# Optimization experiments

Measured on AMD Instinct MI355X. Metric: run time of the kernel, lower is better.

The kernel has to match this reference:

```python
import jax, jax.numpy as jnp
import numpy as np

MOMENTUM = 0.9
COMMITMENT_COST = 0.25
EPS = 1e-20


def setup_inputs() -> dict:
    key = jax.random.key(0)
    k1, k2 = jax.random.split(key)
    D, K = 512, 8192
    B, S = 16, 512
    x = jax.random.normal(k1, (B, S, D), dtype=jnp.float32)
    # variance_scaling(1.0, 'fan_in', 'uniform') on shape (D, K): fan_in = D
    limit = np.sqrt(3.0 / D).astype(np.float32)
    e = jax.random.uniform(k2, (D, K), dtype=jnp.float32, minval=-limit, maxval=limit)
    cs = jnp.zeros((K,), dtype=jnp.float32)
    un = jnp.zeros((D, K), dtype=jnp.float32)
    return {"x": x, "e": e, "cs": cs, "un": un}


def reference(x, e, cs, un):
    D, K = e.shape
    input_shape = x.shape[:-1]            # (B, S)
    xf = x.reshape(-1, D)                 # (N, D)
    # pairwise squared distances: (N, K)
    dist = (jnp.sum(xf * xf, axis=1, keepdims=True)
            + jnp.sum(e * e, axis=0, keepdims=True)
            - 2.0 * xf @ e)
    enc_idx = jnp.argmax(-dist, axis=1)                      # (N,)
    enc = jax.nn.one_hot(enc_idx, K, dtype=x.dtype)          # (N, K)
    quantized = jnp.take(e.T, enc_idx, axis=0).reshape(*input_shape, D)

    # EMA codebook update (train=True branch)
    new_cs = (1.0 - MOMENTUM) * jnp.sum(enc, axis=0) + MOMENTUM * cs
    new_un = (1.0 - MOMENTUM) * (xf.T @ enc) + MOMENTUM * un
    n = jnp.sum(new_cs)
    stable_cs = (new_cs + EPS) / (n + K * EPS) * n
    new_e = new_un / stable_cs[None, :]

    loss = COMMITMENT_COST * jnp.mean((jax.lax.stop_gradient(quantized) - x) ** 2)
    quantized_st = x + jax.lax.stop_gradient(quantized - x)  # straight-through

    avg_probs = jnp.mean(enc.reshape(*input_shape, K), axis=0)           # (S, K)
    over_latents = jnp.mean(avg_probs, axis=tuple(range(len(input_shape) - 1)))  # (K,)
    perplexity = jnp.exp(-jnp.sum(over_latents * jnp.log(over_latents + EPS)))
    return quantized_st, loss, perplexity, enc_idx, new_e, new_cs, new_un
```

## Files before the change

kernel.cpp:

```cpp
#include <hip/hip_runtime.h>
#include <math.h>

#define D_ 512
#define K_ 8192
#define N_ 8192
#define KSLICES 8
#define TAU 0.01f

typedef _Float16 f16x8 __attribute__((ext_vector_type(8)));
typedef __attribute__((ext_vector_type(4))) float f32x4;

__global__ void x2_kernel(const float* __restrict__ x, float* __restrict__ x2f) {
    int n = blockIdx.x * 256 + threadIdx.x;
    const float* row = &x[(size_t)n * D_];
    float b[4];
    #pragma unroll
    for (int blk = 0; blk < 4; ++blk) {
        const float* a = row + blk * 128;
        float r[8];
        #pragma unroll
        for (int j = 0; j < 8; ++j) { float v = a[j]; r[j] = __fmul_rn(v, v); }
        for (int i = 8; i < 128; i += 8) {
            #pragma unroll
            for (int j = 0; j < 8; ++j) {
                float v = a[i + j];
                r[j] = __fadd_rn(r[j], __fmul_rn(v, v));
            }
        }
        b[blk] = __fadd_rn(__fadd_rn(__fadd_rn(r[0], r[1]), __fadd_rn(r[2], r[3])),
                           __fadd_rn(__fadd_rn(r[4], r[5]), __fadd_rn(r[6], r[7])));
    }
    x2f[n] = __fadd_rn(__fadd_rn(b[0], b[1]), __fadd_rn(b[2], b[3]));
}

__global__ void e2f_kernel(const float* __restrict__ e, float* __restrict__ e2f) {
    int k = blockIdx.x * 256 + threadIdx.x;
    float s = 0.0f;
    for (int d = 0; d < D_; ++d) {
        float v = e[(size_t)d * K_ + k];
        s = __fadd_rn(s, __fmul_rn(v, v));
    }
    e2f[k] = s;
}

__global__ void xcvt_kernel(const float* __restrict__ x, _Float16* __restrict__ xf) {
    size_t i = ((size_t)blockIdx.x * 256 + threadIdx.x) * 8;
    float4 a = *(const float4*)&x[i];
    float4 b = *(const float4*)&x[i + 4];
    f16x8 h;
    h[0] = (_Float16)a.x; h[1] = (_Float16)a.y; h[2] = (_Float16)a.z; h[3] = (_Float16)a.w;
    h[4] = (_Float16)b.x; h[5] = (_Float16)b.y; h[6] = (_Float16)b.z; h[7] = (_Float16)b.w;
    *(f16x8*)&xf[i] = h;
}

__global__ void ecvtT_kernel(const float* __restrict__ e, _Float16* __restrict__ efT) {
    __shared__ float t[64][65];
    const int tid = threadIdx.x;
    const int k0 = blockIdx.x * 64;
    const int d0 = blockIdx.y * 64;
    #pragma unroll
    for (int it = 0; it < 4; ++it) {
        int dt = (tid >> 4) + it * 16;
        int c4 = (tid & 15) * 4;
        float4 v = *(const float4*)&e[(size_t)(d0 + dt) * K_ + k0 + c4];
        t[dt][c4 + 0] = v.x; t[dt][c4 + 1] = v.y; t[dt][c4 + 2] = v.z; t[dt][c4 + 3] = v.w;
    }
    __syncthreads();
    const int m = tid >> 2, ch = tid & 3;
    f16x8 h0, h1;
    #pragma unroll
    for (int j = 0; j < 8; ++j) h0[j] = (_Float16)t[ch * 16 + j][m];
    #pragma unroll
    for (int j = 0; j < 8; ++j) h1[j] = (_Float16)t[ch * 16 + 8 + j][m];
    size_t o = (size_t)(k0 + m) * D_ + d0 + ch * 16;
    *(f16x8*)&efT[o] = h0;
    *(f16x8*)&efT[o + 8] = h1;
}

__global__ void etrans_kernel(const float* __restrict__ e, float* __restrict__ eT) {
    __shared__ float t[64][65];
    const int tid = threadIdx.x;
    const int k0 = blockIdx.x * 64;
    const int d0 = blockIdx.y * 64;
    #pragma unroll
    for (int it = 0; it < 4; ++it) {
        int dt = (tid >> 4) + it * 16;
        int c4 = (tid & 15) * 4;
        float4 v = *(const float4*)&e[(size_t)(d0 + dt) * K_ + k0 + c4];
        t[dt][c4 + 0] = v.x; t[dt][c4 + 1] = v.y; t[dt][c4 + 2] = v.z; t[dt][c4 + 3] = v.w;
    }
    __syncthreads();
    const int m = tid >> 2, ch = tid & 3;
    size_t o = (size_t)(k0 + m) * D_ + d0 + ch * 16;
    #pragma unroll
    for (int j4 = 0; j4 < 4; ++j4) {
        float4 w;
        w.x = t[ch * 16 + j4 * 4 + 0][m];
        w.y = t[ch * 16 + j4 * 4 + 1][m];
        w.z = t[ch * 16 + j4 * 4 + 2][m];
        w.w = t[ch * 16 + j4 * 4 + 3][m];
        *(float4*)&eT[o + j4 * 4] = w;
    }
}

__launch_bounds__(256, 2)
__global__ void argmin_mfma(const _Float16* __restrict__ xf, const _Float16* __restrict__ efT,
                            const float* __restrict__ x2f, const float* __restrict__ e2f,
                            float* __restrict__ pv4, int* __restrict__ pi4) {
    __shared__ _Float16 XS[2][4096];
    __shared__ _Float16 ES[2][8192];
    __shared__ float e2s[256];

    const int tid = threadIdx.x;
    const int lane = tid & 63;
    const int wid = tid >> 6;
    const int wm = wid & 1, wn = wid >> 1;
    const int lidx = lane & 15, g = lane >> 4;
    const int rowbase = blockIdx.y * 128;
    const int kslice = blockIdx.x;

    float x2r[4];
    #pragma unroll
    for (int nt = 0; nt < 4; ++nt)
        x2r[nt] = x2f[rowbase + (wn << 6) + (nt << 4) + lidx];

    float best[4], sec[4]; int bi[4], si[4];
    #pragma unroll
    for (int nt = 0; nt < 4; ++nt) {
        best[nt] = 3.0e38f; sec[nt] = 3.0e38f; bi[nt] = 0x7ffffffe; si[nt] = 0x7fffffff;
    }

    const int fx0 = tid,       rx0 = fx0 >> 2, cx0 = ((fx0 & 3) - (rx0 >> 1)) & 3;
    const int fx1 = tid + 256, rx1 = fx1 >> 2, cx1 = ((fx1 & 3) - (rx1 >> 1)) & 3;
    const size_t xo0 = (size_t)(rowbase + rx0) * D_ + cx0 * 8;
    const size_t xo1 = (size_t)(rowbase + rx1) * D_ + cx1 * 8;
    int fe[4], re[4], ce[4];
    #pragma unroll
    for (int j = 0; j < 4; ++j) {
        fe[j] = tid + j * 256; re[j] = fe[j] >> 2; ce[j] = ((fe[j] & 3) - (re[j] >> 1)) & 3;
    }

    for (int cc = 0; cc < 4; ++cc) {
        const int codebase = kslice * 1024 + cc * 256;
        __syncthreads();
        e2s[tid] = e2f[codebase + tid];

        f32x4 acc[8][4];
        const f32x4 z4 = {0.0f, 0.0f, 0.0f, 0.0f};
        #pragma unroll
        for (int mt = 0; mt < 8; ++mt)
            #pragma unroll
            for (int nt = 0; nt < 4; ++nt) acc[mt][nt] = z4;

        f16x8 st[6];
        st[0] = *(const f16x8*)&xf[xo0];
        st[1] = *(const f16x8*)&xf[xo1];
        #pragma unroll
        for (int j = 0; j < 4; ++j)
            st[2 + j] = *(const f16x8*)&efT[(size_t)(codebase + re[j]) * D_ + ce[j] * 8];
        *(f16x8*)&XS[0][fx0 * 8] = st[0];
        *(f16x8*)&XS[0][fx1 * 8] = st[1];
        #pragma unroll
        for (int j = 0; j < 4; ++j) *(f16x8*)&ES[0][fe[j] * 8] = st[2 + j];
        __syncthreads();

        for (int step = 0; step < 16; ++step) {
            const int cur = step & 1;
            if (step < 15) {
                const int d0 = (step + 1) << 5;
                st[0] = *(const f16x8*)&xf[xo0 + d0];
                st[1] = *(const f16x8*)&xf[xo1 + d0];
                #pragma unroll
                for (int j = 0; j < 4; ++j)
                    st[2 + j] = *(const f16x8*)&efT[(size_t)(codebase + re[j]) * D_ + d0 + ce[j] * 8];
            }
            f16x8 bh[4];
            #pragma unroll
            for (int nt = 0; nt < 4; ++nt) {
                int n = (wn << 6) + (nt << 4) + lidx;
                int sb = (g + (n >> 1)) & 3;
                bh[nt] = *(const f16x8*)&XS[cur][n * 32 + sb * 8];
            }
            #pragma unroll
            for (int mt = 0; mt < 8; ++mt) {
                int m = (wm << 7) + (mt << 4) + lidx;
                int sa = (g + (m >> 1)) & 3;
                f16x8 ah = *(const f16x8*)&ES[cur][m * 32 + sa * 8];
                #pragma unroll
                for (int nt = 0; nt < 4; ++nt)
                    acc[mt][nt] = __builtin_amdgcn_mfma_f32_16x16x32_f16(ah, bh[nt], acc[mt][nt], 0, 0, 0);
            }
            if (step < 15) {
                *(f16x8*)&XS[cur ^ 1][fx0 * 8] = st[0];
                *(f16x8*)&XS[cur ^ 1][fx1 * 8] = st[1];
                #pragma unroll
                for (int j = 0; j < 4; ++j) *(f16x8*)&ES[cur ^ 1][fe[j] * 8] = st[2 + j];
            }
            __syncthreads();
        }

        #pragma unroll
        for (int mt = 0; mt < 8; ++mt) {
            #pragma unroll
            for (int r = 0; r < 4; ++r) {
                const int ml = (wm << 7) + (mt << 4) + (g << 2) + r;
                const float e2k = e2s[ml];
                const int kg = codebase + ml;
                #pragma unroll
                for (int nt = 0; nt < 4; ++nt) {
                    float dot = acc[mt][nt][r];
                    float s = __fsub_rn(__fadd_rn(x2r[nt], e2k), __fmul_rn(2.0f, dot));
                    if (s < best[nt]) {
                        sec[nt] = best[nt]; si[nt] = bi[nt];
                        best[nt] = s; bi[nt] = kg;
                    } else if (s < sec[nt]) {
                        sec[nt] = s; si[nt] = kg;
                    }
                }
            }
        }
    }

    __syncthreads();
    float* entV = (float*)XS;
    int*   entI = (int*)ES;
    #pragma unroll
    for (int nt = 0; nt < 4; ++nt) {
        int rl = (wn << 6) + (nt << 4) + lidx;
        int slot = ((wm << 2) + g) << 1;
        entV[rl * 16 + slot] = best[nt];  entI[rl * 16 + slot] = bi[nt];
        entV[rl * 16 + slot + 1] = sec[nt]; entI[rl * 16 + slot + 1] = si[nt];
    }
    __syncthreads();
    if (tid < 128) {
        float v4[4] = {3.0e38f, 3.0e38f, 3.0e38f, 3.0e38f};
        int i4[4] = {0x7fffffff, 0x7fffffff, 0x7fffffff, 0x7fffffff};
        #pragma unroll
        for (int t2 = 0; t2 < 16; ++t2) {
            float v = entV[tid * 16 + t2]; int i = entI[tid * 16 + t2];
            #pragma unroll
            for (int p = 0; p < 4; ++p) {
                bool better = (v < v4[p]) || (v == v4[p] && i < i4[p]);
                if (better) {
                    float tv = v4[p]; v4[p] = v; v = tv;
                    int ti = i4[p]; i4[p] = i; i = ti;
                }
            }
        }
        size_t o = (size_t)(rowbase + tid) * 32 + kslice * 4;
        #pragma unroll
        for (int p = 0; p < 4; ++p) { pv4[o + p] = v4[p]; pi4[o + p] = i4[p]; }
    }
}

__global__ void argmin_reduce(const float* __restrict__ pv4, const int* __restrict__ pi4,
                              int* __restrict__ idxbuf, float* __restrict__ out_idx,
                              int* __restrict__ flaglist, unsigned* __restrict__ nflag) {
    int n = blockIdx.x * 256 + threadIdx.x;
    float bv = 3.0e38f, sv = 3.0e38f; int bi = 0x7fffffff;
    for (int j = 0; j < 32; ++j) {
        float v = pv4[(size_t)n * 32 + j]; int i = pi4[(size_t)n * 32 + j];
        if (v < bv || (v == bv && i < bi)) { sv = bv; bv = v; bi = i; }
        else if (v < sv) sv = v;
    }
    idxbuf[n] = bi;
    out_idx[n] = (float)bi;
    if (sv - bv < TAU) {
        unsigned pos = atomicAdd(nflag, 1u);
        flaglist[pos] = n;
    }
}

__launch_bounds__(256, 2)
__global__ void refine_kernel(const float* __restrict__ x, const float* __restrict__ e,
                              const float* __restrict__ x2f, const float* __restrict__ e2f,
                              const int* __restrict__ flaglist, const unsigned* __restrict__ nflag,
                              const float* __restrict__ pv4, const int* __restrict__ pi4,
                              int* __restrict__ idxbuf, float* __restrict__ out_idx) {
    __shared__ float xrow[D_];
    __shared__ double part[32][8];
    __shared__ int candi[32];
    __shared__ float sv[32];
    const int tid = threadIdx.x;
    const unsigned nf = *nflag;
    for (unsigned f = blockIdx.x; f < nf; f += gridDim.x) {
        const int n = flaglist[f];
        __syncthreads();
        if (tid < 32) candi[tid] = pi4[(size_t)n * 32 + tid];
        for (int d = tid; d < D_; d += 256) xrow[d] = x[(size_t)n * D_ + d];
        __syncthreads();
        const int c = tid >> 3, j = tid & 7;
        const int k = candi[c];
        double a = 0.0;
        #pragma unroll 8
        for (int d = j; d < D_; d += 8)
            a = fma((double)xrow[d], (double)e[(size_t)d * K_ + k], a);
        part[c][j] = a;
        __syncthreads();
        if (j == 0) {
            double dot = ((part[c][0] + part[c][1]) + (part[c][2] + part[c][3]))
                       + ((part[c][4] + part[c][5]) + (part[c][6] + part[c][7]));
            float md = (float)dot;
            sv[c] = __fsub_rn(__fadd_rn(x2f[n], e2f[k]), __fmul_rn(2.0f, md));
        }
        __syncthreads();
        if (tid == 0) {
            float bv = 3.0e38f; int bi = 0x7fffffff;
            for (int c2 = 0; c2 < 32; ++c2) {
                float v = sv[c2]; int i2 = candi[c2];
                if (v < bv || (v == bv && i2 < bi)) { bv = v; bi = i2; }
            }
            idxbuf[n] = bi; out_idx[n] = (float)bi;
        }
        __syncthreads();
    }
}

__global__ void counts_kernel(const int* __restrict__ idxbuf, unsigned* __restrict__ counts) {
    int n = blockIdx.x * 256 + threadIdx.x;
    atomicAdd(&counts[idxbuf[n]], 1u);
}

__global__ void scan_kernel(const unsigned* __restrict__ counts,
                            unsigned* __restrict__ offsets, unsigned* __restrict__ cursor) {
    __shared__ unsigned ps[256];
    const int t = threadIdx.x;
    const int base = t * 32;
    unsigned s = 0;
    for (int j = 0; j < 32; ++j) s += counts[base + j];
    ps[t] = s;
    __syncthreads();
    for (int off = 1; off < 256; off <<= 1) {
        unsigned v = (t >= off) ? ps[t - off] : 0u;
        __syncthreads();
        ps[t] += v;
        __syncthreads();
    }
    unsigned run = (t > 0) ? ps[t - 1] : 0u;
    for (int j = 0; j < 32; ++j) {
        int k = base + j;
        offsets[k] = run;
        cursor[k] = run;
        run += counts[k];
    }
}

__global__ void fill_kernel(const int* __restrict__ idxbuf, unsigned* __restrict__ cursor,
                            int* __restrict__ rowlist) {
    int n = blockIdx.x * 256 + threadIdx.x;
    int k = idxbuf[n];
    unsigned pos = atomicAdd(&cursor[k], 1u);
    rowlist[pos] = n;
}

__global__ void quant_loss_kernel(const float* __restrict__ x, const float* __restrict__ eT,
                                  const int* __restrict__ idxbuf,
                                  float* __restrict__ qout, double* __restrict__ loss_part) {
    int n = blockIdx.x;
    int k = idxbuf[n];
    int d = threadIdx.x * 2;
    float2 q = *(const float2*)&eT[(size_t)k * D_ + d];
    float2 xv = *(const float2*)&x[(size_t)n * D_ + d];
    float2 o;
    float dfx = q.x - xv.x, dfy = q.y - xv.y;
    o.x = xv.x + dfx; o.y = xv.y + dfy;
    *(float2*)&qout[(size_t)n * D_ + d] = o;
    double part = fma((double)dfx, (double)dfx, (double)dfy * (double)dfy);
    __shared__ double sr[256];
    sr[threadIdx.x] = part;
    __syncthreads();
    for (int s = 128; s > 0; s >>= 1) {
        if (threadIdx.x < s) sr[threadIdx.x] += sr[threadIdx.x + s];
        __syncthreads();
    }
    if (threadIdx.x == 0) loss_part[n] = sr[0];
}

__global__ void cs_kernel(const unsigned* __restrict__ counts, const float* __restrict__ cs,
                          float* __restrict__ out_cs,
                          double* __restrict__ ncs_part, double* __restrict__ ent_part) {
    int tid = threadIdx.x;
    int k = blockIdx.x * 256 + tid;
    float cnt = (float)counts[k];
    float ncs = 0.1f * cnt + 0.9f * cs[k];
    out_cs[k] = ncs;
    double p = (double)counts[k] / 8192.0;
    double ent = -p * log(p + 1e-20);

    __shared__ double s1[256], s2[256];
    s1[tid] = (double)ncs;
    s2[tid] = ent;
    __syncthreads();
    for (int s = 128; s > 0; s >>= 1) {
        if (tid < s) { s1[tid] += s1[tid + s]; s2[tid] += s2[tid + s]; }
        __syncthreads();
    }
    if (tid == 0) { ncs_part[blockIdx.x] = s1[0]; ent_part[blockIdx.x] = s2[0]; }
}

__global__ void scalars_kernel(const double* __restrict__ loss_part,
                               const double* __restrict__ ncs_part,
                               const double* __restrict__ ent_part,
                               float* __restrict__ out_loss, float* __restrict__ out_ppl,
                               double* __restrict__ nsum_out) {
    __shared__ double sr[256];
    double s = 0.0;
    for (int i = threadIdx.x; i < N_; i += 256) s += loss_part[i];
    sr[threadIdx.x] = s;
    __syncthreads();
    for (int t = 128; t > 0; t >>= 1) {
        if (threadIdx.x < t) sr[threadIdx.x] += sr[threadIdx.x + t];
        __syncthreads();
    }
    if (threadIdx.x == 0) {
        out_loss[0] = (float)(0.25 * (sr[0] / (double)((size_t)N_ * D_)));
        double nsum = 0.0, ent = 0.0;
        for (int i = 0; i < 32; ++i) { nsum += ncs_part[i]; ent += ent_part[i]; }
        out_ppl[0] = (float)exp(ent);
        nsum_out[0] = nsum;
    }
}

__global__ void merge_kernel(const float* __restrict__ x, const float* __restrict__ un,
                             const float* __restrict__ out_cs,
                             const unsigned* __restrict__ offsets, const unsigned* __restrict__ counts,
                             const int* __restrict__ rowlist, const double* __restrict__ nsum,
                             float* __restrict__ out_un, float* __restrict__ out_e) {
    const int f = blockIdx.x * 256 + threadIdx.x;
    const int k = f & (K_ - 1);
    const int d0 = (f >> 13) * 4;
    const unsigned start = offsets[k];
    const unsigned cnt = counts[k];
    float4 s = {0.0f, 0.0f, 0.0f, 0.0f};
    for (unsigned i = 0; i < cnt; ++i) {
        int nr = rowlist[start + i];
        const float4 v = *(const float4*)&x[(size_t)nr * D_ + d0];
        s.x += v.x; s.y += v.y; s.z += v.z; s.w += v.w;
    }
    const double nn = nsum[0];
    const double denom = nn + 8192.0 * 1e-20;
    const float scs = (float)((((double)out_cs[k] + 1e-20) / denom) * nn);
    const float sv[4] = {s.x, s.y, s.z, s.w};
    #pragma unroll
    for (int j = 0; j < 4; ++j) {
        size_t o = (size_t)(d0 + j) * K_ + k;
        float uval = 0.9f * un[o] + 0.1f * sv[j];
        out_un[o] = uval;
        out_e[o] = uval / scs;
    }
}

extern "C" void kernel_launch(void* const* d_in, const int* in_sizes, int n_in,
                              void* d_out, int out_size, void* d_ws, size_t ws_size,
                              hipStream_t stream) {
    const float* x  = (const float*)d_in[0];
    const float* e  = (const float*)d_in[1];
    const float* cs = (const float*)d_in[2];
    const float* un = (const float*)d_in[3];

    float* out = (float*)d_out;
    float* out_q    = out;
    float* out_loss = out + 4194304;
    float* out_ppl  = out + 4194305;
    float* out_idx  = out + 4194306;
    float* out_e    = out + 4202498;
    float* out_cs   = out + 8396802;
    float* out_un   = out + 8404994;

    _Float16* xf16 = (_Float16*)out_q;
    _Float16* efT  = (_Float16*)out_e;
    float* pv4 = (float*)out_un;
    int*   pi4 = (int*)(out_un + 262144);
    float* eTf32 = (float*)out_un;

    char* ws = (char*)d_ws;
    unsigned* counts  = (unsigned*)ws;
    unsigned* nflag   = (unsigned*)(ws + 32768);
    float* x2f        = (float*)(ws + 36864);
    float* e2f        = (float*)(ws + 69632);
    int*   idxbuf     = (int*)(ws + 102400);
    int*   flaglist   = (int*)(ws + 135168);
    double* loss_part = (double*)(ws + 167936);
    double* ncs_part  = (double*)(ws + 233472);
    double* ent_part  = (double*)(ws + 233728);
    double* nsum      = (double*)(ws + 233984);
    unsigned* offsets = (unsigned*)(ws + 234240);
    unsigned* cursor  = (unsigned*)(ws + 267008);
    int*   rowlist    = (int*)(ws + 299776);

    hipMemsetAsync(d_ws, 0, 36864, stream);
    xcvt_kernel<<<2048, 256, 0, stream>>>(x, xf16);
    ecvtT_kernel<<<dim3(K_ / 64, D_ / 64), 256, 0, stream>>>(e, efT);
    x2_kernel<<<N_ / 256, 256, 0, stream>>>(x, x2f);
    e2f_kernel<<<K_ / 256, 256, 0, stream>>>(e, e2f);
    argmin_mfma<<<dim3(KSLICES, N_ / 128), 256, 0, stream>>>(xf16, efT, x2f, e2f, pv4, pi4);
    argmin_reduce<<<N_ / 256, 256, 0, stream>>>(pv4, pi4, idxbuf, out_idx, flaglist, nflag);
    refine_kernel<<<256, 256, 0, stream>>>(x, e, x2f, e2f, flaglist, nflag, pv4, pi4, idxbuf, out_idx);
    etrans_kernel<<<dim3(K_ / 64, D_ / 64), 256, 0, stream>>>(e, eTf32);
    counts_kernel<<<N_ / 256, 256, 0, stream>>>(idxbuf, counts);
    scan_kernel<<<1, 256, 0, stream>>>(counts, offsets, cursor);
    fill_kernel<<<N_ / 256, 256, 0, stream>>>(idxbuf, cursor, rowlist);
    quant_loss_kernel<<<N_, 256, 0, stream>>>(x, eTf32, idxbuf, out_q, loss_part);
    cs_kernel<<<K_ / 256, 256, 0, stream>>>(counts, cs, out_cs, ncs_part, ent_part);
    scalars_kernel<<<1, 256, 0, stream>>>(loss_part, ncs_part, ent_part, out_loss, out_ppl, nsum);
    merge_kernel<<<K_ * (D_ / 4) / 256, 256, 0, stream>>>(x, un, out_cs, offsets, counts, rowlist, nsum, out_un, out_e);
}
```

Before: 261.6 us.

## Fuse fp16 and fp32 codebook transposes into one kernel, refine via transposed codebook

Merges the fp16 transposed-codebook conversion and the fp32 transpose into a single eprep kernel, so the codebook is read and staged through shared memory once instead of twice. The argmin partial buffers move into the quantized-output region so the fp32 transposed codebook can live in out_un from the start. The refine kernel then reads contiguous rows of the transposed codebook instead of strided columns. Also shrinks the x2/e2f blocks to 64 threads for more blocks, unrolls the e2f loop, and uses nontemporal loads for x tiles in the MFMA argmin. Buffer aliasing gets more intricate, so it depends on the pv4/pi4 region not overlapping the fp16 x copy.

New measurement: 271.0 us. 3.6% more time.

```diff
diff --git a/kernel.cpp b/kernel.cpp
--- a/kernel.cpp
+++ b/kernel.cpp
@@ -11,7 +11,7 @@
 typedef __attribute__((ext_vector_type(4))) float f32x4;
 
 __global__ void x2_kernel(const float* __restrict__ x, float* __restrict__ x2f) {
-    int n = blockIdx.x * 256 + threadIdx.x;
+    int n = blockIdx.x * 64 + threadIdx.x;
     const float* row = &x[(size_t)n * D_];
     float b[4];
     #pragma unroll
@@ -34,8 +34,9 @@
 }
 
 __global__ void e2f_kernel(const float* __restrict__ e, float* __restrict__ e2f) {
-    int k = blockIdx.x * 256 + threadIdx.x;
+    int k = blockIdx.x * 64 + threadIdx.x;
     float s = 0.0f;
+    #pragma unroll 4
     for (int d = 0; d < D_; ++d) {
         float v = e[(size_t)d * K_ + k];
         s = __fadd_rn(s, __fmul_rn(v, v));
@@ -53,7 +54,8 @@
     *(f16x8*)&xf[i] = h;
 }
 
-__global__ void ecvtT_kernel(const float* __restrict__ e, _Float16* __restrict__ efT) {
+__global__ void eprep_kernel(const float* __restrict__ e,
+                             _Float16* __restrict__ efT, float* __restrict__ eT) {
     __shared__ float t[64][65];
     const int tid = threadIdx.x;
     const int k0 = blockIdx.x * 64;
@@ -67,31 +69,14 @@
     }
     __syncthreads();
     const int m = tid >> 2, ch = tid & 3;
+    size_t o = (size_t)(k0 + m) * D_ + d0 + ch * 16;
     f16x8 h0, h1;
     #pragma unroll
     for (int j = 0; j < 8; ++j) h0[j] = (_Float16)t[ch * 16 + j][m];
     #pragma unroll
     for (int j = 0; j < 8; ++j) h1[j] = (_Float16)t[ch * 16 + 8 + j][m];
-    size_t o = (size_t)(k0 + m) * D_ + d0 + ch * 16;
     *(f16x8*)&efT[o] = h0;
     *(f16x8*)&efT[o + 8] = h1;
-}
-
-__global__ void etrans_kernel(const float* __restrict__ e, float* __restrict__ eT) {
-    __shared__ float t[64][65];
-    const int tid = threadIdx.x;
-    const int k0 = blockIdx.x * 64;
-    const int d0 = blockIdx.y * 64;
-    #pragma unroll
-    for (int it = 0; it < 4; ++it) {
-        int dt = (tid >> 4) + it * 16;
-        int c4 = (tid & 15) * 4;
-        float4 v = *(const float4*)&e[(size_t)(d0 + dt) * K_ + k0 + c4];
-        t[dt][c4 + 0] = v.x; t[dt][c4 + 1] = v.y; t[dt][c4 + 2] = v.z; t[dt][c4 + 3] = v.w;
-    }
-    __syncthreads();
-    const int m = tid >> 2, ch = tid & 3;
-    size_t o = (size_t)(k0 + m) * D_ + d0 + ch * 16;
     #pragma unroll
     for (int j4 = 0; j4 < 4; ++j4) {
         float4 w;
@@ -153,8 +138,8 @@
             for (int nt = 0; nt < 4; ++nt) acc[mt][nt] = z4;
 
         f16x8 st[6];
-        st[0] = *(const f16x8*)&xf[xo0];
-        st[1] = *(const f16x8*)&xf[xo1];
+        st[0] = __builtin_nontemporal_load((const f16x8*)&xf[xo0]);
+        st[1] = __builtin_nontemporal_load((const f16x8*)&xf[xo1]);
         #pragma unroll
         for (int j = 0; j < 4; ++j)
             st[2 + j] = *(const f16x8*)&efT[(size_t)(codebase + re[j]) * D_ + ce[j] * 8];
@@ -168,8 +153,8 @@
             const int cur = step & 1;
             if (step < 15) {
                 const int d0 = (step + 1) << 5;
-                st[0] = *(const f16x8*)&xf[xo0 + d0];
-                st[1] = *(const f16x8*)&xf[xo1 + d0];
+                st[0] = __builtin_nontemporal_load((const f16x8*)&xf[xo0 + d0]);
+                st[1] = __builtin_nontemporal_load((const f16x8*)&xf[xo1 + d0]);
                 #pragma unroll
                 for (int j = 0; j < 4; ++j)
                     st[2 + j] = *(const f16x8*)&efT[(size_t)(codebase + re[j]) * D_ + d0 + ce[j] * 8];
@@ -272,10 +257,10 @@
 }
 
 __launch_bounds__(256, 2)
-__global__ void refine_kernel(const float* __restrict__ x, const float* __restrict__ e,
+__global__ void refine_kernel(const float* __restrict__ x, const float* __restrict__ eT,
                               const float* __restrict__ x2f, const float* __restrict__ e2f,
                               const int* __restrict__ flaglist, const unsigned* __restrict__ nflag,
-                              const float* __restrict__ pv4, const int* __restrict__ pi4,
+                              const int* __restrict__ pi4,
                               int* __restrict__ idxbuf, float* __restrict__ out_idx) {
     __shared__ float xrow[D_];
     __shared__ double part[32][8];
@@ -294,7 +279,7 @@
         double a = 0.0;
         #pragma unroll 8
         for (int d = j; d < D_; d += 8)
-            a = fma((double)xrow[d], (double)e[(size_t)d * K_ + k], a);
+            a = fma((double)xrow[d], (double)eT[(size_t)k * D_ + d], a);
         part[c][j] = a;
         __syncthreads();
         if (j == 0) {
@@ -468,10 +453,10 @@
     float* out_un   = out + 8404994;
 
     _Float16* xf16 = (_Float16*)out_q;
+    float* pv4 = (float*)(out_q + 2097152);
+    int*   pi4 = (int*)(out_q + 2359296);
     _Float16* efT  = (_Float16*)out_e;
-    float* pv4 = (float*)out_un;
-    int*   pi4 = (int*)(out_un + 262144);
-    float* eTf32 = (float*)out_un;
+    float* eT = (float*)out_un;
 
     char* ws = (char*)d_ws;
     unsigned* counts  = (unsigned*)ws;
@@ -490,17 +475,16 @@
 
     hipMemsetAsync(d_ws, 0, 36864, stream);
     xcvt_kernel<<<2048, 256, 0, stream>>>(x, xf16);
-    ecvtT_kernel<<<dim3(K_ / 64, D_ / 64), 256, 0, stream>>>(e, efT);
-    x2_kernel<<<N_ / 256, 256, 0, stream>>>(x, x2f);
-    e2f_kernel<<<K_ / 256, 256, 0, stream>>>(e, e2f);
+    eprep_kernel<<<dim3(K_ / 64, D_ / 64), 256, 0, stream>>>(e, efT, eT);
+    x2_kernel<<<N_ / 64, 64, 0, stream>>>(x, x2f);
+    e2f_kernel<<<K_ / 64, 64, 0, stream>>>(e, e2f);
     argmin_mfma<<<dim3(KSLICES, N_ / 128), 256, 0, stream>>>(xf16, efT, x2f, e2f, pv4, pi4);
     argmin_reduce<<<N_ / 256, 256, 0, stream>>>(pv4, pi4, idxbuf, out_idx, flaglist, nflag);
-    refine_kernel<<<256, 256, 0, stream>>>(x, e, x2f, e2f, flaglist, nflag, pv4, pi4, idxbuf, out_idx);
-    etrans_kernel<<<dim3(K_ / 64, D_ / 64), 256, 0, stream>>>(e, eTf32);
+    refine_kernel<<<256, 256, 0, stream>>>(x, eT, x2f, e2f, flaglist, nflag, pi4, idxbuf, out_idx);
     counts_kernel<<<N_ / 256, 256, 0, stream>>>(idxbuf, counts);
     scan_kernel<<<1, 256, 0, stream>>>(counts, offsets, cursor);
     fill_kernel<<<N_ / 256, 256, 0, stream>>>(idxbuf, cursor, rowlist);
-    quant_loss_kernel<<<N_, 256, 0, stream>>>(x, eTf32, idxbuf, out_q, loss_part);
+    quant_loss_kernel<<<N_, 256, 0, stream>>>(x, eT, idxbuf, out_q, loss_part);
     cs_kernel<<<K_ / 256, 256, 0, stream>>>(counts, cs, out_cs, ncs_part, ent_part);
     scalars_kernel<<<1, 256, 0, stream>>>(loss_part, ncs_part, ent_part, out_loss, out_ppl, nsum);
     merge_kernel<<<K_ * (D_ / 4) / 256, 256, 0, stream>>>(x, un, out_cs, offsets, counts, rowlist, nsum, out_un, out_e);
```
